# Kernel optimization log

Hardware: AMD Instinct MI355X
Metric: run time of the kernel (lower is better)

Reference implementation:

```python
import jax, jax.numpy as jnp
import numpy as np
import math

B, C, D, H, DFF, K = 32, 512, 512, 8, 2048, 7
EPS = 1e-6
DN = ('NCH', 'OIH', 'NCH')


def causal_conv(x, w, b):
    # x: (B, C, D); conv over last axis, left pad K-1 (causal)
    y = jax.lax.conv_general_dilated(x, w, window_strides=(1,),
                                     padding=[(K - 1, 0)], dimension_numbers=DN)
    return y + b[None, :, None]


def layer_norm(x, g, b):
    # torch: mean / unbiased std over last dim; gamma*(x-mean)/(std+eps)+beta
    mean = x.mean(-1, keepdims=True)
    var = x.var(-1, ddof=1, keepdims=True)
    return g * (x - mean) / (jnp.sqrt(var) + EPS) + b


def mha(q_in, kv, wq, bq, wk, bk, wv, bv, wo, bo):
    dh = D // H
    q = causal_conv(q_in, wq, bq)
    k = causal_conv(kv, wk, bk)
    v = causal_conv(kv, wv, bv)
    # split feature dim D into heads; sequence axis is C
    def split(t):
        return t.reshape(B, C, H, dh).transpose(0, 2, 1, 3)  # (B,H,C,dh)
    qh, kh, vh = split(q), split(k), split(v)
    scores = jnp.einsum('bhqd,bhkd->bhqk', qh, kh) / math.sqrt(dh)
    p = jax.nn.softmax(scores, axis=-1)
    o = jnp.einsum('bhqk,bhkd->bhqd', p, vh)          # (B,H,C,dh)
    o = o.transpose(0, 2, 1, 3).reshape(B, C, D)
    return causal_conv(o, wo, bo)


def setup_inputs() -> dict:
    key = jax.random.key(0)
    ks = jax.random.split(key, 12)
    s_conv = 1.0 / math.sqrt(C * K)
    s_lin1 = 1.0 / math.sqrt(D)
    s_lin2 = 1.0 / math.sqrt(DFF)
    return {
        'x': jax.random.normal(ks[0], (B, C, D), jnp.float32),
        'w_conv_in': jax.random.normal(ks[1], (C, C, K), jnp.float32) * s_conv,
        'b_conv_in': jnp.zeros((C,), jnp.float32),
        'wq': jax.random.normal(ks[2], (C, C, K), jnp.float32) * s_conv,
        'bq': jnp.zeros((C,), jnp.float32),
        'wk': jax.random.normal(ks[3], (C, C, K), jnp.float32) * s_conv,
        'bk': jnp.zeros((C,), jnp.float32),
        'wv': jax.random.normal(ks[4], (C, C, K), jnp.float32) * s_conv,
        'bv': jnp.zeros((C,), jnp.float32),
        'wo': jax.random.normal(ks[5], (C, C, K), jnp.float32) * s_conv,
        'bo': jnp.zeros((C,), jnp.float32),
        'ln0_g': jnp.ones((D,), jnp.float32),
        'ln0_b': jnp.zeros((D,), jnp.float32),
        'ln1_g': jnp.ones((D,), jnp.float32),
        'ln1_b': jnp.zeros((D,), jnp.float32),
        'w1': jax.random.normal(ks[6], (D, DFF), jnp.float32) * s_lin1,
        'b1': jnp.zeros((DFF,), jnp.float32),
        'w2': jax.random.normal(ks[7], (DFF, D), jnp.float32) * s_lin2,
        'b2': jnp.zeros((D,), jnp.float32),
    }


def reference(x, w_conv_in, b_conv_in, wq, bq, wk, bk, wv, bv, wo, bo,
              ln0_g, ln0_b, ln1_g, ln1_b, w1, b1, w2, b2):
    # EncoderLayer.forward (eval mode: dropout = identity)
    query_in = causal_conv(x, w_conv_in, b_conv_in)
    xn = layer_norm(query_in, ln0_g, ln0_b)
    # SublayerOutput: y = sublayer(norm(x)); return y + dropout(y)  (= 2y eval)
    y = mha(query_in, xn, wq, bq, wk, bk, wv, bv, wo, bo)
    h1 = y + y
    # FFN sublayer, same residual pattern
    hn = layer_norm(h1, ln1_g, ln1_b)
    ff = jnp.einsum('bcf,fd->bcd', jax.nn.relu(jnp.einsum('bcd,df->bcf', hn, w1) + b1), w2) + b2
    return ff + ff
```

## Files before the change

kernel.cpp:

```cpp
#include <hip/hip_runtime.h>
#include <hip/hip_bf16.h>

typedef __hip_bfloat16 bf16;
typedef __attribute__((ext_vector_type(8))) short short8;
typedef __attribute__((ext_vector_type(4))) float floatx4;

#define NB 32
#define NC 512
#define ND 512
#define NDH 64
#define NFF 2048
#define KW 7

__device__ __forceinline__ float bf2f(bf16 v) { return __bfloat162float(v); }
__device__ __forceinline__ bf16 f2bf(float f) { return __float2bfloat16(f); }

typedef __attribute__((address_space(3))) unsigned lds_u32;
typedef __attribute__((address_space(1))) const unsigned glb_u32;
__device__ __forceinline__ void async_copy16(void* lds_dst, const void* gsrc) {
  __builtin_amdgcn_global_load_lds((glb_u32*)gsrc, (lds_u32*)lds_dst, 16, 0, 0);
}

__global__ __launch_bounds__(256) void k_transpose_w(const float* __restrict__ w,
                                                     bf16* __restrict__ wt) {
  int idx = blockIdx.x * 256 + threadIdx.x;
  if (idx >= NC * NC) return;
  int co = idx >> 9, ci = idx & 511;
#pragma unroll
  for (int t = 0; t < KW; ++t)
    wt[(size_t)t * NC * NC + co * NC + ci] = f2bf(w[(size_t)co * NC * KW + (size_t)ci * KW + t]);
}

__global__ __launch_bounds__(256) void k_transpose2d(const float* __restrict__ src,
                                                     bf16* __restrict__ dst,
                                                     int R, int Ccols) {
  __shared__ bf16 t[32][33];
  int bc = blockIdx.x * 32, br = blockIdx.y * 32;
  size_t so = (size_t)blockIdx.z * R * Ccols;
  int tx = threadIdx.x & 31, ty = threadIdx.x >> 5;
#pragma unroll
  for (int i = 0; i < 32; i += 8)
    t[ty + i][tx] = f2bf(src[so + (size_t)(br + ty + i) * Ccols + bc + tx]);
  __syncthreads();
#pragma unroll
  for (int i = 0; i < 32; i += 8)
    dst[so + (size_t)(bc + ty + i) * R + br + tx] = t[tx][ty + i];
}

template <bool TRANS_OUT>
__global__ __launch_bounds__(256, 3) void k_conv(const bf16* __restrict__ Xt,
                                                 const bf16* __restrict__ Wt,
                                                 const float* __restrict__ bias,
                                                 bf16* __restrict__ Y, float outScale,
                                                 const bf16* __restrict__ zp) {
  __shared__ __align__(16) bf16 Ws[512 * 32];
  __shared__ __align__(16) bf16 Xs[144 * 32];
  const int d0 = blockIdx.x * 128;
  const int co0 = blockIdx.y * 128;
  const int b = blockIdx.z;
  const int tid = threadIdx.x, lane = tid & 63, wave = tid >> 6;
  const int m16 = lane & 15, qd = lane >> 4;
  const int wm = (wave & 1) * 64, wn = (wave >> 1) * 64;
  const int l4 = lane >> 2;
  const int seg = (lane & 3) ^ ((l4 >> 1) & 3);

  const bf16* xb = Xt + (size_t)b * ND * NC;
  const bf16* pw = Wt + (size_t)(co0 + l4) * NC + seg * 8;
  const bf16* pxm = xb + (ptrdiff_t)(d0 - 6 + l4) * NC + seg * 8;
  const bf16* px0 = (d0 == 0 && l4 < 6) ? (zp + seg * 8) : pxm;
  const bf16* px8 = (d0 == 384 && l4 >= 6) ? (zp + seg * 8) : pxm;

  floatx4 acc[4][4];
  const floatx4 zero = {0.f, 0.f, 0.f, 0.f};
#pragma unroll
  for (int i = 0; i < 4; ++i)
#pragma unroll
    for (int j = 0; j < 4; ++j) acc[i][j] = zero;

  const int physW = qd ^ ((m16 >> 1) & 3);

  for (int cs = 0; cs < 16; ++cs) {
    const int ko = cs * 32;
    __syncthreads();
    {
      const bf16* s0 = (wave == 0) ? px0 : pxm;
      async_copy16(Xs + wave * 512, s0 + wave * (16 * NC) + ko);
      async_copy16(Xs + (wave + 4) * 512, pxm + (wave + 4) * (16 * NC) + ko);
      if (wave == 0) async_copy16(Xs + 8 * 512, px8 + 8 * (16 * NC) + ko);
      const bf16* pt = pw + (size_t)wave * NC * NC + ko;
#pragma unroll
      for (int q = 0; q < 8; ++q)
        async_copy16(Ws + (wave * 8 + q) * 512, pt + q * (16 * NC));
    }
    __syncthreads();
#pragma unroll
    for (int t = 0; t < 4; ++t) {
      short8 wf[4], xf[4];
#pragma unroll
      for (int i = 0; i < 4; ++i)
        wf[i] = *reinterpret_cast<const short8*>(Ws + (t * 128 + wm + i * 16 + m16) * 32 + physW * 8);
      int rb = wn + m16 + t;
      int physX = qd ^ ((rb >> 1) & 3);
#pragma unroll
      for (int j = 0; j < 4; ++j)
        xf[j] = *reinterpret_cast<const short8*>(Xs + (rb + j * 16) * 32 + physX * 8);
#pragma unroll
      for (int i = 0; i < 4; ++i)
#pragma unroll
        for (int j = 0; j < 4; ++j)
          acc[i][j] = TRANS_OUT
              ? __builtin_amdgcn_mfma_f32_16x16x32_bf16(xf[j], wf[i], acc[i][j], 0, 0, 0)
              : __builtin_amdgcn_mfma_f32_16x16x32_bf16(wf[i], xf[j], acc[i][j], 0, 0, 0);
    }
    __syncthreads();
#pragma unroll
    for (int k = 0; k < 6; ++k) {
      int s = wave * 6 + k;
      int tl = s >> 3, q = s & 7;
      async_copy16(Ws + s * 512, pw + (size_t)(tl + 4) * NC * NC + q * (16 * NC) + ko);
    }
    __syncthreads();
#pragma unroll
    for (int tl = 0; tl < 3; ++tl) {
      short8 wf[4], xf[4];
#pragma unroll
      for (int i = 0; i < 4; ++i)
        wf[i] = *reinterpret_cast<const short8*>(Ws + (tl * 128 + wm + i * 16 + m16) * 32 + physW * 8);
      int rb = wn + m16 + tl + 4;
      int physX = qd ^ ((rb >> 1) & 3);
#pragma unroll
      for (int j = 0; j < 4; ++j)
        xf[j] = *reinterpret_cast<const short8*>(Xs + (rb + j * 16) * 32 + physX * 8);
#pragma unroll
      for (int i = 0; i < 4; ++i)
#pragma unroll
        for (int j = 0; j < 4; ++j)
          acc[i][j] = TRANS_OUT
              ? __builtin_amdgcn_mfma_f32_16x16x32_bf16(xf[j], wf[i], acc[i][j], 0, 0, 0)
              : __builtin_amdgcn_mfma_f32_16x16x32_bf16(wf[i], xf[j], acc[i][j], 0, 0, 0);
    }
  }

  if (!TRANS_OUT) {
    bf16* yb = Y + (size_t)b * NC * ND;
#pragma unroll
    for (int i = 0; i < 4; ++i) {
      int cobase = co0 + wm + i * 16 + qd * 4;
#pragma unroll
      for (int j = 0; j < 4; ++j) {
        int dcol = d0 + wn + j * 16 + m16;
#pragma unroll
        for (int r = 0; r < 4; ++r) {
          float v = (acc[i][j][r] + bias[cobase + r]) * outScale;
          yb[(size_t)(cobase + r) * ND + dcol] = f2bf(v);
        }
      }
    }
  } else {
    bf16* yb = Y + (size_t)b * ND * NC;
#pragma unroll
    for (int i = 0; i < 4; ++i) {
      int ccol = co0 + wm + i * 16 + m16;
      float bv = bias[ccol];
#pragma unroll
      for (int j = 0; j < 4; ++j) {
        int drow = d0 + wn + j * 16 + qd * 4;
#pragma unroll
        for (int r = 0; r < 4; ++r) {
          float v = (acc[i][j][r] + bv) * outScale;
          yb[(size_t)(drow + r) * NC + ccol] = f2bf(v);
        }
      }
    }
  }
}

__global__ __launch_bounds__(256, 4) void k_layernorm(const bf16* __restrict__ x,
                                                      const float* __restrict__ gamma,
                                                      const float* __restrict__ beta,
                                                      bf16* __restrict__ y) {
  int row = blockIdx.x * 4 + (threadIdx.x >> 6);
  int lane = threadIdx.x & 63;
  const bf16* xr = x + (size_t)row * ND + lane * 8;
  uint4 raw = *reinterpret_cast<const uint4*>(xr);
  const bf16* rp = reinterpret_cast<const bf16*>(&raw);
  float v[8];
#pragma unroll
  for (int j = 0; j < 8; ++j) v[j] = bf2f(rp[j]);
  float s = 0.f;
#pragma unroll
  for (int j = 0; j < 8; ++j) s += v[j];
#pragma unroll
  for (int m = 32; m >= 1; m >>= 1) s += __shfl_xor(s, m, 64);
  float mean = s * (1.f / 512.f);
  float ss = 0.f;
#pragma unroll
  for (int j = 0; j < 8; ++j) { float dd = v[j] - mean; ss += dd * dd; }
#pragma unroll
  for (int m = 32; m >= 1; m >>= 1) ss += __shfl_xor(ss, m, 64);
  float rden = 1.f / (sqrtf(ss * (1.f / 511.f)) + 1e-6f);
  __align__(16) bf16 outv[8];
#pragma unroll
  for (int j = 0; j < 8; ++j)
    outv[j] = f2bf(gamma[lane * 8 + j] * (v[j] - mean) * rden + beta[lane * 8 + j]);
  *reinterpret_cast<uint4*>(y + (size_t)row * ND + lane * 8) = *reinterpret_cast<uint4*>(outv);
}

__global__ __launch_bounds__(256, 2) void k_layernorm_col(const bf16* __restrict__ x,
                                                          const float* __restrict__ gamma,
                                                          const float* __restrict__ beta,
                                                          bf16* __restrict__ y) {
  __shared__ float red[2][8][256];
  __shared__ float mS[256], rS[256];
  const int b = blockIdx.y;
  const int c0 = blockIdx.x * 256;
  const int t = threadIdx.x;
  const int g = t & 31, sl = t >> 5;
  const bf16* xb = x + (size_t)b * ND * NC + c0 + g * 8;
  float fs[8], fq[8];
#pragma unroll
  for (int j = 0; j < 8; ++j) { fs[j] = 0.f; fq[j] = 0.f; }
  for (int i = 0; i < 64; ++i) {
    int r = sl * 64 + i;
    uint4 raw = *reinterpret_cast<const uint4*>(xb + (size_t)r * NC);
    const bf16* rp = reinterpret_cast<const bf16*>(&raw);
#pragma unroll
    for (int j = 0; j < 8; ++j) { float v = bf2f(rp[j]); fs[j] += v; fq[j] += v * v; }
  }
#pragma unroll
  for (int j = 0; j < 8; ++j) { red[0][sl][g * 8 + j] = fs[j]; red[1][sl][g * 8 + j] = fq[j]; }
  __syncthreads();
  {
    float s = 0.f, q = 0.f;
#pragma unroll
    for (int s2 = 0; s2 < 8; ++s2) { s += red[0][s2][t]; q += red[1][s2][t]; }
    float mean = s * (1.f / 512.f);
    float var = fmaxf((q - 512.f * mean * mean) * (1.f / 511.f), 0.f);
    mS[t] = mean;
    rS[t] = 1.f / (sqrtf(var) + 1e-6f);
  }
  __syncthreads();
  float mv[8], rv[8];
#pragma unroll
  for (int j = 0; j < 8; ++j) { mv[j] = mS[g * 8 + j]; rv[j] = rS[g * 8 + j]; }
  bf16* yb = y + (size_t)b * ND * NC + c0 + g * 8;
  for (int i = 0; i < 64; ++i) {
    int r = sl * 64 + i;
    uint4 raw = *reinterpret_cast<const uint4*>(xb + (size_t)r * NC);
    const bf16* rp = reinterpret_cast<const bf16*>(&raw);
    float gr = gamma[r], br = beta[r];
    __align__(16) bf16 ov[8];
#pragma unroll
    for (int j = 0; j < 8; ++j) ov[j] = f2bf(gr * (bf2f(rp[j]) - mv[j]) * rv[j] + br);
    *reinterpret_cast<uint4*>(yb + (size_t)r * NC) = *reinterpret_cast<uint4*>(ov);
  }
}

__global__ __launch_bounds__(256, 3) void k_attention(const bf16* __restrict__ Q,
                                                      const bf16* __restrict__ K,
                                                      const bf16* __restrict__ Vt,
                                                      bf16* __restrict__ OT) {
  __shared__ __align__(16) bf16 Ks[64 * 64];
  __shared__ __align__(16) bf16 Ps[4][32][72];
  __shared__ float linvS[4][32];
  const int qc = blockIdx.x, h = blockIdx.y, b = blockIdx.z;
  const int tid = threadIdx.x, lane = tid & 63, wave = tid >> 6;
  const int m16 = lane & 15, qd = lane >> 4;
  const size_t base = (size_t)b * NC * ND;
  const size_t baseT = (size_t)b * ND * NC;

  short8 aq[2][2];
#pragma unroll
  for (int ms = 0; ms < 2; ++ms)
#pragma unroll
    for (int ks = 0; ks < 2; ++ks)
      aq[ms][ks] = *reinterpret_cast<const short8*>(
          Q + base + (size_t)(qc * 128 + wave * 32 + ms * 16 + m16) * ND + h * 64 + ks * 32 + qd * 8);

  const bf16* kg[2];
  bf16* kl[2];
#pragma unroll
  for (int s = 0; s < 2; ++s) {
    int i = wave * 2 + s;
    int row = i * 8 + (lane >> 3);
    int sg = (lane & 7) ^ (row & 7);
    kg[s] = K + base + (size_t)row * ND + h * 64 + sg * 8;
    kl[s] = Ks + i * 512;
  }

  floatx4 oa[4][2];
  const floatx4 zero = {0.f, 0.f, 0.f, 0.f};
#pragma unroll
  for (int i = 0; i < 4; ++i)
#pragma unroll
    for (int j = 0; j < 2; ++j) oa[i][j] = zero;
  float lsum[2][4];
#pragma unroll
  for (int i = 0; i < 2; ++i)
#pragma unroll
    for (int r = 0; r < 4; ++r) lsum[i][r] = 0.f;

  for (int kc = 0; kc < 8; ++kc) {
    __syncthreads();
#pragma unroll
    for (int s = 0; s < 2; ++s) async_copy16(kl[s], kg[s] + (size_t)(kc * 64) * ND);
    __syncthreads();
    floatx4 sc[2][4];
#pragma unroll
    for (int i = 0; i < 2; ++i)
#pragma unroll
      for (int j = 0; j < 4; ++j) sc[i][j] = zero;
#pragma unroll
    for (int ks = 0; ks < 2; ++ks)
#pragma unroll
      for (int n = 0; n < 4; ++n) {
        int row = n * 16 + m16;
        int phys = (ks * 4 + qd) ^ (row & 7);
        short8 bk = *reinterpret_cast<const short8*>(Ks + row * 64 + phys * 8);
#pragma unroll
        for (int ms = 0; ms < 2; ++ms)
          sc[ms][n] = __builtin_amdgcn_mfma_f32_16x16x32_bf16(aq[ms][ks], bk, sc[ms][n], 0, 0, 0);
      }
#pragma unroll
    for (int ms = 0; ms < 2; ++ms)
#pragma unroll
      for (int n = 0; n < 4; ++n)
#pragma unroll
        for (int r = 0; r < 4; ++r) {
          float p = __expf(sc[ms][n][r] * 0.125f);
          lsum[ms][r] += p;
          Ps[wave][ms * 16 + qd * 4 + r][n * 16 + m16] = f2bf(p);
        }
#pragma unroll
    for (int ks = 0; ks < 2; ++ks) {
      short8 bp[2];
#pragma unroll
      for (int j = 0; j < 2; ++j)
        bp[j] = *reinterpret_cast<const short8*>(&Ps[wave][j * 16 + m16][ks * 32 + qd * 8]);
#pragma unroll
      for (int i = 0; i < 4; ++i) {
        short8 av = *reinterpret_cast<const short8*>(
            Vt + baseT + (size_t)(h * 64 + i * 16 + m16) * NC + kc * 64 + ks * 32 + qd * 8);
#pragma unroll
        for (int j = 0; j < 2; ++j)
          oa[i][j] = __builtin_amdgcn_mfma_f32_16x16x32_bf16(av, bp[j], oa[i][j], 0, 0, 0);
      }
    }
  }
#pragma unroll
  for (int ms = 0; ms < 2; ++ms)
#pragma unroll
    for (int r = 0; r < 4; ++r) {
      float t = lsum[ms][r];
      t += __shfl_xor(t, 1, 64);
      t += __shfl_xor(t, 2, 64);
      t += __shfl_xor(t, 4, 64);
      t += __shfl_xor(t, 8, 64);
      if (m16 == 0) linvS[wave][ms * 16 + qd * 4 + r] = 1.f / t;
    }
  __syncthreads();
  float lsc[2];
#pragma unroll
  for (int j = 0; j < 2; ++j) lsc[j] = linvS[wave][j * 16 + m16];
#pragma unroll
  for (int i = 0; i < 4; ++i) {
    int drow = h * 64 + i * 16 + qd * 4;
#pragma unroll
    for (int j = 0; j < 2; ++j) {
      int qcol = qc * 128 + wave * 32 + j * 16 + m16;
#pragma unroll
      for (int r = 0; r < 4; ++r)
        OT[baseT + (size_t)(drow + r) * NC + qcol] = f2bf(oa[i][j][r] * lsc[j]);
    }
  }
}

__global__ __launch_bounds__(256, 3) void k_gemm_bt(const bf16* __restrict__ A,
                                                    const bf16* __restrict__ Bt,
                                                    const float* __restrict__ bias,
                                                    void* __restrict__ Y,
                                                    int Kdim, int Ndim, int mode) {
  __shared__ __align__(16) bf16 As[128 * 32];
  __shared__ __align__(16) bf16 Bs[128 * 32];
  const int n0 = blockIdx.x * 128, m0 = blockIdx.y * 128;
  const int tid = threadIdx.x, lane = tid & 63, wave = tid >> 6;
  const int wm = (wave & 1) * 64, wn = (wave >> 1) * 64;
  const int m16 = lane & 15, qd = lane >> 4;

  const bf16* gb[4];
  bf16* lb[4];
#pragma unroll
  for (int idx = 0; idx < 4; ++idx) {
    int s = wave + idx * 4;
    int which = s >> 3;
    int i8 = s & 7;
    int row = i8 * 16 + (lane >> 2);
    int sg = (lane & 3) ^ ((row >> 1) & 3);
    const bf16* src = which ? (Bt + (size_t)(n0 + row) * Kdim) : (A + (size_t)(m0 + row) * Kdim);
    gb[idx] = src + sg * 8;
    lb[idx] = (which ? Bs : As) + i8 * 512;
  }

  floatx4 acc[4][4];
  const floatx4 zero = {0.f, 0.f, 0.f, 0.f};
#pragma unroll
  for (int i = 0; i < 4; ++i)
#pragma unroll
    for (int j = 0; j < 4; ++j) acc[i][j] = zero;

  for (int ks = 0; ks < Kdim / 32; ++ks) {
    __syncthreads();
#pragma unroll
    for (int idx = 0; idx < 4; ++idx) async_copy16(lb[idx], gb[idx] + ks * 32);
    __syncthreads();
    short8 af[4], bfv[4];
#pragma unroll
    for (int i = 0; i < 4; ++i) {
      int ra = wm + i * 16 + m16;
      af[i] = *reinterpret_cast<const short8*>(As + ra * 32 + (qd ^ ((ra >> 1) & 3)) * 8);
      int rb = wn + i * 16 + m16;
      bfv[i] = *reinterpret_cast<const short8*>(Bs + rb * 32 + (qd ^ ((rb >> 1) & 3)) * 8);
    }
#pragma unroll
    for (int j = 0; j < 4; ++j)
#pragma unroll
      for (int i = 0; i < 4; ++i)
        acc[i][j] = __builtin_amdgcn_mfma_f32_16x16x32_bf16(af[i], bfv[j], acc[i][j], 0, 0, 0);
  }
#pragma unroll
  for (int i = 0; i < 4; ++i) {
    int m = m0 + wm + i * 16 + qd * 4;
#pragma unroll
    for (int j = 0; j < 4; ++j) {
      int n = n0 + wn + j * 16 + m16;
      float bv = bias[n];
#pragma unroll
      for (int r = 0; r < 4; ++r) {
        float v = acc[i][j][r] + bv;
        size_t idx = (size_t)(m + r) * Ndim + n;
        if (mode == 0)
          ((bf16*)Y)[idx] = f2bf(fmaxf(v, 0.f));
        else
          ((float*)Y)[idx] = 2.f * v;
      }
    }
  }
}

extern "C" void kernel_launch(void* const* d_in, const int* in_sizes, int n_in,
                              void* d_out, int out_size, void* d_ws, size_t ws_size,
                              hipStream_t stream) {
  (void)in_sizes; (void)n_in; (void)out_size; (void)ws_size;
  const float* x         = (const float*)d_in[0];
  const float* w_conv_in = (const float*)d_in[1];
  const float* b_conv_in = (const float*)d_in[2];
  const float* wq        = (const float*)d_in[3];
  const float* bq        = (const float*)d_in[4];
  const float* wk        = (const float*)d_in[5];
  const float* bk        = (const float*)d_in[6];
  const float* wv        = (const float*)d_in[7];
  const float* bv        = (const float*)d_in[8];
  const float* wo        = (const float*)d_in[9];
  const float* bo        = (const float*)d_in[10];
  const float* ln0_g     = (const float*)d_in[11];
  const float* ln0_b     = (const float*)d_in[12];
  const float* ln1_g     = (const float*)d_in[13];
  const float* ln1_b     = (const float*)d_in[14];
  const float* w1        = (const float*)d_in[15];
  const float* b1        = (const float*)d_in[16];
  const float* w2        = (const float*)d_in[17];
  const float* b2        = (const float*)d_in[18];

  char* ws = (char*)d_ws;
  const size_t ZP  = 262144;
  const size_t WT  = (size_t)KW * NC * NC * 2;
  const size_t W1T = (size_t)NFF * ND * 2;
  const size_t ACT = (size_t)NB * NC * ND * 2;
  size_t off = 0;
  bf16* zp    = (bf16*)(ws + off); off += ZP;
  bf16* wt_in = (bf16*)(ws + off); off += WT;
  bf16* wt_q  = (bf16*)(ws + off); off += WT;
  bf16* wt_k  = (bf16*)(ws + off); off += WT;
  bf16* wt_v  = (bf16*)(ws + off); off += WT;
  bf16* wt_o  = (bf16*)(ws + off); off += WT;
  bf16* w1t   = (bf16*)(ws + off); off += W1T;
  bf16* w2t   = (bf16*)(ws + off); off += W1T;
  bf16* T1    = (bf16*)(ws + off); off += ACT;
  bf16* T2    = (bf16*)(ws + off); off += ACT;
  bf16* T3    = (bf16*)(ws + off); off += ACT;
  bf16* T4    = (bf16*)(ws + off); off += ACT;
  bf16* T5    = (bf16*)(ws + off); off += ACT;
  bf16* mid   = (bf16*)(ws + off); off += (size_t)NB * NC * NFF * 2;

  hipMemsetAsync(zp, 0, ZP, stream);

  k_transpose_w<<<1024, 256, 0, stream>>>(w_conv_in, wt_in);
  k_transpose_w<<<1024, 256, 0, stream>>>(wq, wt_q);
  k_transpose_w<<<1024, 256, 0, stream>>>(wk, wt_k);
  k_transpose_w<<<1024, 256, 0, stream>>>(wv, wt_v);
  k_transpose_w<<<1024, 256, 0, stream>>>(wo, wt_o);
  k_transpose2d<<<dim3(NFF / 32, ND / 32, 1), 256, 0, stream>>>(w1, w1t, ND, NFF);
  k_transpose2d<<<dim3(ND / 32, NFF / 32, 1), 256, 0, stream>>>(w2, w2t, NFF, ND);
  k_transpose2d<<<dim3(ND / 32, NC / 32, NB), 256, 0, stream>>>(x, T1, NC, ND);

  dim3 cgrid(ND / 128, NC / 128, NB);
  k_conv<true><<<cgrid, 256, 0, stream>>>(T1, wt_in, b_conv_in, T2, 1.f, zp);
  k_layernorm_col<<<dim3(NC / 256, NB), 256, 0, stream>>>(T2, ln0_g, ln0_b, T3);
  k_conv<false><<<cgrid, 256, 0, stream>>>(T2, wt_q, bq, T4, 1.f, zp);
  k_conv<false><<<cgrid, 256, 0, stream>>>(T3, wt_k, bk, T1, 1.f, zp);
  k_conv<true><<<cgrid, 256, 0, stream>>>(T3, wt_v, bv, T5, 1.f, zp);
  k_attention<<<dim3(NC / 128, 8, NB), 256, 0, stream>>>(T4, T1, T5, T3);
  k_conv<false><<<cgrid, 256, 0, stream>>>(T3, wt_o, bo, T4, 2.f, zp);
  k_layernorm<<<NB * NC / 4, 256, 0, stream>>>(T4, ln1_g, ln1_b, T2);
  k_gemm_bt<<<dim3(NFF / 128, NB * NC / 128), 256, 0, stream>>>(T2, w1t, b1, mid, ND, NFF, 0);
  k_gemm_bt<<<dim3(ND / 128, NB * NC / 128), 256, 0, stream>>>(mid, w2t, b2, d_out, NFF, ND, 1);
}
```

Baseline: 638.8 us.

## Merge weight transposes, widen layernorm_col grid, stage V tiles in LDS

Three separate changes. The five conv-weight transposes become one kernel that stages each output-channel row in shared memory, replacing strided global reads with coalesced loads. The column layernorm now uses 64-column blocks, giving four times as many blocks and fully unrolled row loops for better occupancy. The attention kernel copies V tiles into a swizzled LDS buffer asynchronously next to the K tiles instead of reading V directly from global memory in the PV MFMA loop, at the cost of 8 KB more shared memory per block.

```diff
diff --git a/kernel.cpp b/kernel.cpp
--- a/kernel.cpp
+++ b/kernel.cpp
@@ -21,14 +21,30 @@
   __builtin_amdgcn_global_load_lds((glb_u32*)gsrc, (lds_u32*)lds_dst, 16, 0, 0);
 }
 
-__global__ __launch_bounds__(256) void k_transpose_w(const float* __restrict__ w,
-                                                     bf16* __restrict__ wt) {
-  int idx = blockIdx.x * 256 + threadIdx.x;
-  if (idx >= NC * NC) return;
-  int co = idx >> 9, ci = idx & 511;
-#pragma unroll
-  for (int t = 0; t < KW; ++t)
-    wt[(size_t)t * NC * NC + co * NC + ci] = f2bf(w[(size_t)co * NC * KW + (size_t)ci * KW + t]);
+__global__ __launch_bounds__(256) void k_transpose_w_all(
+    const float* __restrict__ w0, const float* __restrict__ w1,
+    const float* __restrict__ w2, const float* __restrict__ w3,
+    const float* __restrict__ w4, bf16* __restrict__ t0, bf16* __restrict__ t1,
+    bf16* __restrict__ t2, bf16* __restrict__ t3, bf16* __restrict__ t4) {
+  __shared__ float row[NC * KW];
+  const int co = blockIdx.x;
+  const int which = blockIdx.y;
+  const float* w = which == 0 ? w0 : which == 1 ? w1 : which == 2 ? w2 : which == 3 ? w3 : w4;
+  bf16* wt = which == 0 ? t0 : which == 1 ? t1 : which == 2 ? t2 : which == 3 ? t3 : t4;
+  const int tid = threadIdx.x;
+  const float* src = w + (size_t)co * NC * KW;
+#pragma unroll
+  for (int i = 0; i < 14; ++i) row[tid + i * 256] = src[tid + i * 256];
+  __syncthreads();
+  const int ci = tid * 2;
+#pragma unroll
+  for (int t = 0; t < KW; ++t) {
+    bf16 a = f2bf(row[ci * KW + t]);
+    bf16 b = f2bf(row[ci * KW + KW + t]);
+    bf16* dst = wt + (size_t)t * NC * NC + (size_t)co * NC + ci;
+    dst[0] = a;
+    dst[1] = b;
+  }
 }
 
 __global__ __launch_bounds__(256) void k_transpose2d(const float* __restrict__ src,
@@ -206,22 +222,23 @@
   *reinterpret_cast<uint4*>(y + (size_t)row * ND + lane * 8) = *reinterpret_cast<uint4*>(outv);
 }
 
-__global__ __launch_bounds__(256, 2) void k_layernorm_col(const bf16* __restrict__ x,
+__global__ __launch_bounds__(256, 4) void k_layernorm_col(const bf16* __restrict__ x,
                                                           const float* __restrict__ gamma,
                                                           const float* __restrict__ beta,
                                                           bf16* __restrict__ y) {
-  __shared__ float red[2][8][256];
-  __shared__ float mS[256], rS[256];
+  __shared__ float red[2][32][64];
+  __shared__ float mS[64], rS[64];
   const int b = blockIdx.y;
-  const int c0 = blockIdx.x * 256;
+  const int c0 = blockIdx.x * 64;
   const int t = threadIdx.x;
-  const int g = t & 31, sl = t >> 5;
+  const int g = t & 7, sl = t >> 3;
   const bf16* xb = x + (size_t)b * ND * NC + c0 + g * 8;
   float fs[8], fq[8];
 #pragma unroll
   for (int j = 0; j < 8; ++j) { fs[j] = 0.f; fq[j] = 0.f; }
-  for (int i = 0; i < 64; ++i) {
-    int r = sl * 64 + i;
+#pragma unroll
+  for (int i = 0; i < 16; ++i) {
+    int r = sl * 16 + i;
     uint4 raw = *reinterpret_cast<const uint4*>(xb + (size_t)r * NC);
     const bf16* rp = reinterpret_cast<const bf16*>(&raw);
 #pragma unroll
@@ -230,10 +247,10 @@
 #pragma unroll
   for (int j = 0; j < 8; ++j) { red[0][sl][g * 8 + j] = fs[j]; red[1][sl][g * 8 + j] = fq[j]; }
   __syncthreads();
-  {
+  if (t < 64) {
     float s = 0.f, q = 0.f;
 #pragma unroll
-    for (int s2 = 0; s2 < 8; ++s2) { s += red[0][s2][t]; q += red[1][s2][t]; }
+    for (int s2 = 0; s2 < 32; ++s2) { s += red[0][s2][t]; q += red[1][s2][t]; }
     float mean = s * (1.f / 512.f);
     float var = fmaxf((q - 512.f * mean * mean) * (1.f / 511.f), 0.f);
     mS[t] = mean;
@@ -244,8 +261,9 @@
 #pragma unroll
   for (int j = 0; j < 8; ++j) { mv[j] = mS[g * 8 + j]; rv[j] = rS[g * 8 + j]; }
   bf16* yb = y + (size_t)b * ND * NC + c0 + g * 8;
-  for (int i = 0; i < 64; ++i) {
-    int r = sl * 64 + i;
+#pragma unroll
+  for (int i = 0; i < 16; ++i) {
+    int r = sl * 16 + i;
     uint4 raw = *reinterpret_cast<const uint4*>(xb + (size_t)r * NC);
     const bf16* rp = reinterpret_cast<const bf16*>(&raw);
     float gr = gamma[r], br = beta[r];
@@ -261,6 +279,7 @@
                                                       const bf16* __restrict__ Vt,
                                                       bf16* __restrict__ OT) {
   __shared__ __align__(16) bf16 Ks[64 * 64];
+  __shared__ __align__(16) bf16 Vs[64 * 64];
   __shared__ __align__(16) bf16 Ps[4][32][72];
   __shared__ float linvS[4][32];
   const int qc = blockIdx.x, h = blockIdx.y, b = blockIdx.z;
@@ -279,6 +298,8 @@
 
   const bf16* kg[2];
   bf16* kl[2];
+  const bf16* vg[2];
+  bf16* vl[2];
 #pragma unroll
   for (int s = 0; s < 2; ++s) {
     int i = wave * 2 + s;
@@ -286,6 +307,8 @@
     int sg = (lane & 7) ^ (row & 7);
     kg[s] = K + base + (size_t)row * ND + h * 64 + sg * 8;
     kl[s] = Ks + i * 512;
+    vg[s] = Vt + baseT + (size_t)(h * 64 + row) * NC + sg * 8;
+    vl[s] = Vs + i * 512;
   }
 
   floatx4 oa[4][2];
@@ -303,7 +326,10 @@
   for (int kc = 0; kc < 8; ++kc) {
     __syncthreads();
 #pragma unroll
-    for (int s = 0; s < 2; ++s) async_copy16(kl[s], kg[s] + (size_t)(kc * 64) * ND);
+    for (int s = 0; s < 2; ++s) {
+      async_copy16(kl[s], kg[s] + (size_t)(kc * 64) * ND);
+      async_copy16(vl[s], vg[s] + kc * 64);
+    }
     __syncthreads();
     floatx4 sc[2][4];
 #pragma unroll
@@ -339,8 +365,9 @@
         bp[j] = *reinterpret_cast<const short8*>(&Ps[wave][j * 16 + m16][ks * 32 + qd * 8]);
 #pragma unroll
       for (int i = 0; i < 4; ++i) {
-        short8 av = *reinterpret_cast<const short8*>(
-            Vt + baseT + (size_t)(h * 64 + i * 16 + m16) * NC + kc * 64 + ks * 32 + qd * 8);
+        int row = i * 16 + m16;
+        int phys = (ks * 4 + qd) ^ (row & 7);
+        short8 av = *reinterpret_cast<const short8*>(Vs + row * 64 + phys * 8);
 #pragma unroll
         for (int j = 0; j < 2; ++j)
           oa[i][j] = __builtin_amdgcn_mfma_f32_16x16x32_bf16(av, bp[j], oa[i][j], 0, 0, 0);
@@ -494,18 +521,15 @@
 
   hipMemsetAsync(zp, 0, ZP, stream);
 
-  k_transpose_w<<<1024, 256, 0, stream>>>(w_conv_in, wt_in);
-  k_transpose_w<<<1024, 256, 0, stream>>>(wq, wt_q);
-  k_transpose_w<<<1024, 256, 0, stream>>>(wk, wt_k);
-  k_transpose_w<<<1024, 256, 0, stream>>>(wv, wt_v);
-  k_transpose_w<<<1024, 256, 0, stream>>>(wo, wt_o);
+  k_transpose_w_all<<<dim3(NC, 5), 256, 0, stream>>>(
+      w_conv_in, wq, wk, wv, wo, wt_in, wt_q, wt_k, wt_v, wt_o);
   k_transpose2d<<<dim3(NFF / 32, ND / 32, 1), 256, 0, stream>>>(w1, w1t, ND, NFF);
   k_transpose2d<<<dim3(ND / 32, NFF / 32, 1), 256, 0, stream>>>(w2, w2t, NFF, ND);
   k_transpose2d<<<dim3(ND / 32, NC / 32, NB), 256, 0, stream>>>(x, T1, NC, ND);
 
   dim3 cgrid(ND / 128, NC / 128, NB);
   k_conv<true><<<cgrid, 256, 0, stream>>>(T1, wt_in, b_conv_in, T2, 1.f, zp);
-  k_layernorm_col<<<dim3(NC / 256, NB), 256, 0, stream>>>(T2, ln0_g, ln0_b, T3);
+  k_layernorm_col<<<dim3(NC / 64, NB), 256, 0, stream>>>(T2, ln0_g, ln0_b, T3);
   k_conv<false><<<cgrid, 256, 0, stream>>>(T2, wt_q, bq, T4, 1.f, zp);
   k_conv<false><<<cgrid, 256, 0, stream>>>(T3, wt_k, bk, T1, 1.f, zp);
   k_conv<true><<<cgrid, 256, 0, stream>>>(T3, wt_v, bv, T5, 1.f, zp);
```

New measurement: 570.7 us. 1.12x faster.
